# Optimization experiments

Measured on AMD Instinct MI355X. Metric: run time of the kernel, lower is better.

Reference implementation:

```python
import jax, jax.numpy as jnp
import numpy as np

EPS = 1e-7            # keras.backend.epsilon()
NEG = -1e30           # log-space 'zero' (avoid -inf for NaN-free grads)
SUB_SAMPLE = (2, 2)   # encoder conv subsampling factors (non-tensor forward arg)


def setup_inputs() -> dict:
    key = jax.random.key(0)
    k1, k2, k3, k4 = jax.random.split(key, 4)
    B, T, C, L = 128, 2000, 128, 200
    logits = jax.random.normal(k1, (B, T, C), jnp.float32)
    y_pred = jax.nn.softmax(logits, axis=-1)  # ctc_batch_cost expects probabilities
    labels = jax.random.randint(k2, (B, L), 0, C - 1, jnp.int32)  # never the blank (C-1)
    # raw frame counts; after two /2 subsamplings -> in [1000, 2000] <= T
    feat_lens = jax.random.randint(k3, (B,), 4000, 8000, jnp.int32)
    label_lens = jax.random.randint(k4, (B,), 50, L + 1, jnp.int32)
    return {"y_pred": y_pred, "labels": labels, "feat_lens": feat_lens, "label_lens": label_lens}


def _ctc_batch_cost(y_pred, labels, feat_lens, label_lens):
    """Faithful reimplementation of keras.backend.ctc_batch_cost (blank = C-1),
    with the CTCLayer's subsampling of feat_lens applied first."""
    for sub in SUB_SAMPLE:
        if sub > 1:
            feat_lens = (feat_lens + 1) // sub
    log_probs = jnp.log(y_pred + EPS)                 # [B,T,C]
    B, T, C = y_pred.shape
    L = labels.shape[1]
    S = 2 * L + 1
    blank = C - 1

    # extended label sequence: blank, l1, blank, l2, ..., blank  -> [B,S]
    ext = jnp.full((B, S), blank, jnp.int32).at[:, 1::2].set(labels)
    # skip transition s-2 -> s allowed iff ext[s] != blank and ext[s] != ext[s-2]
    skip_ok = jnp.concatenate(
        [jnp.zeros((B, 2), bool), (ext[:, 2:] != blank) & (ext[:, 2:] != ext[:, :-2])],
        axis=1,
    )
    bidx = jnp.arange(B)
    i1 = 2 * label_lens - 1   # last non-blank state
    i2 = 2 * label_lens       # trailing blank state

    lp = jnp.swapaxes(log_probs, 0, 1)                # [T,B,C], scan over time

    emit0 = jnp.take_along_axis(lp[0], ext, axis=1)   # [B,S]
    alpha0 = (jnp.full((B, S), NEG, jnp.float32)
              .at[:, 0].set(emit0[:, 0])
              .at[:, 1].set(emit0[:, 1]))
    ll0 = jnp.logaddexp(alpha0[bidx, i1], alpha0[bidx, i2])
    final0 = jnp.where(feat_lens == 1, ll0, NEG)

    def step(carry, inp):
        alpha, final = carry
        t, lp_t = inp
        emit = jnp.take_along_axis(lp_t, ext, axis=1)              # [B,S]
        a1 = jnp.pad(alpha, ((0, 0), (1, 0)), constant_values=NEG)[:, :-1]
        a2 = jnp.pad(alpha, ((0, 0), (2, 0)), constant_values=NEG)[:, :-2]
        m = jnp.logaddexp(alpha, a1)
        m = jnp.where(skip_ok, jnp.logaddexp(m, a2), m)
        alpha = m + emit
        ll = jnp.logaddexp(alpha[bidx, i1], alpha[bidx, i2])
        final = jnp.where(t == feat_lens - 1, ll, final)           # capture at last valid frame
        return (alpha, final), None

    (_, final), _ = jax.lax.scan(step, (alpha0, final0), (jnp.arange(1, T), lp[1:]))
    return -final[:, None]                                          # [B,1] like ctc_batch_cost


def reference(y_pred, labels, feat_lens, label_lens):
    return _ctc_batch_cost(y_pred, labels, feat_lens, label_lens)
```

## Files before the change

kernel.cpp:

```cpp
#include <hip/hip_runtime.h>
#include <math.h>

#define EPSQ 1e-7f
#define TDIM 2000
#define CDIM 128
#define LDIM 200
#define SDIM 401
#define SPL  7
#define SENTE (-(1 << 30))

#define RINGA 0
#define RINGB 8192
#define LABSI 16384
#define PRODA 16592
#define CONSA 16593
#define PRODB 16594
#define CONSB 16595
#define BDONE 16596
#define BVALS 16608
#define BEXPI 17056
#define SMEMN 17120

__device__ __forceinline__ float dpp_shr_f(float x) {
    return __int_as_float(__builtin_amdgcn_update_dpp(0, __float_as_int(x), 0x138, 0xf, 0xf, true));
}
__device__ __forceinline__ int dpp_shr_i(int x) {
    return __builtin_amdgcn_update_dpp(0, x, 0x138, 0xf, 0xf, true);
}
__device__ __forceinline__ float dpp_shl_f(float x) {
    return __int_as_float(__builtin_amdgcn_update_dpp(0, __float_as_int(x), 0x130, 0xf, 0xf, true));
}
__device__ __forceinline__ int dpp_shl_i(int x) {
    return __builtin_amdgcn_update_dpp(0, x, 0x130, 0xf, 0xf, true);
}

__device__ __forceinline__ void renorm_alpha(float a[SPL], int& E, float& fprev, int lane) {
    float mx = fmaxf(fmaxf(fmaxf(a[0], a[1]), fmaxf(a[2], a[3])),
                     fmaxf(fmaxf(a[4], a[5]), a[6]));
    bool zero = (mx == 0.f);
    int e = ((__float_as_int(mx) >> 23) & 0xff) - 127;
    int S_self = zero ? SENTE : (E + e);
    int S1 = dpp_shr_i(S_self);
    if (lane == 0) S1 = SENTE;
    int S2 = dpp_shr_i(S1);
    if (lane == 0) S2 = SENTE;
    int E_new = max(S_self, S1);
    int E_prevnew = max(S1, S2);
    int dg = E - E_new;
    float g = (zero || dg < -126) ? 0.f : __int_as_float((dg + 127) << 23);
#pragma unroll
    for (int j = 0; j < SPL; ++j) a[j] *= g;
    E = E_new;
    int df = E_prevnew - E_new;
    bool fz = (E_prevnew <= SENTE / 2) || (df < -126);
    if (df > 126) df = 126;
    fprev = fz ? 0.f : __int_as_float((df + 127) << 23);
}

__device__ __forceinline__ void renorm_beta(float b[SPL], int& E, float& fnext, int lane) {
    float mx = fmaxf(fmaxf(fmaxf(b[0], b[1]), fmaxf(b[2], b[3])),
                     fmaxf(fmaxf(b[4], b[5]), b[6]));
    bool zero = (mx == 0.f);
    int e = ((__float_as_int(mx) >> 23) & 0xff) - 127;
    int S_self = zero ? SENTE : (E + e);
    int S1 = dpp_shl_i(S_self);
    if (lane == 63) S1 = SENTE;
    int S2 = dpp_shl_i(S1);
    if (lane == 63) S2 = SENTE;
    int E_new = max(S_self, S1);
    int E_nextnew = max(S1, S2);
    int dg = E - E_new;
    float g = (zero || dg < -126) ? 0.f : __int_as_float((dg + 127) << 23);
#pragma unroll
    for (int j = 0; j < SPL; ++j) b[j] *= g;
    E = E_new;
    int df = E_nextnew - E_new;
    bool fz = (E_nextnew <= SENTE / 2) || (df < -126);
    if (df > 126) df = 126;
    fnext = fz ? 0.f : __int_as_float((df + 127) << 23);
}

#define A_STEP(TOFF) do {                                                     \
    float p6 = dpp_shr_f(a[6]) * fprev;                                       \
    float p5 = dpp_shr_f(a[5]) * fprev;                                       \
    float n0 = fmaf(skipf[0], p5,   a[0] + p6)   * q[(1+(TOFF))&3][0];        \
    float n1 = fmaf(skipf[1], p6,   a[1] + a[0]) * q[(1+(TOFF))&3][1];        \
    float n2 = fmaf(skipf[2], a[0], a[2] + a[1]) * q[(1+(TOFF))&3][2];        \
    float n3 = fmaf(skipf[3], a[1], a[3] + a[2]) * q[(1+(TOFF))&3][3];        \
    float n4 = fmaf(skipf[4], a[2], a[4] + a[3]) * q[(1+(TOFF))&3][4];        \
    float n5 = fmaf(skipf[5], a[3], a[5] + a[4]) * q[(1+(TOFF))&3][5];        \
    float n6 = fmaf(skipf[6], a[4], a[6] + a[5]) * q[(1+(TOFF))&3][6];        \
    a[0]=n0; a[1]=n1; a[2]=n2; a[3]=n3; a[4]=n4; a[5]=n5; a[6]=n6;            \
    if (t + (TOFF) == m) {                                                    \
        _Pragma("unroll")                                                     \
        for (int j = 0; j < SPL; ++j) ac[j] = a[j];                           \
        Eac = E;                                                              \
    }                                                                         \
    {   const int rr = ((t + (TOFF) + 2) & 63) << 7;                          \
        _Pragma("unroll")                                                     \
        for (int j = 0; j < SPL; ++j)                                         \
            q[(3+(TOFF))&3][j] = ringA[rr + cls[j]];                          \
    }                                                                         \
} while (0);

#define B_STEP(SOFF) do {                                                     \
    float c0 = bb[0]*q[(SOFF)&3][0], c1 = bb[1]*q[(SOFF)&3][1];               \
    float c2 = bb[2]*q[(SOFF)&3][2], c3 = bb[3]*q[(SOFF)&3][3];               \
    float c4 = bb[4]*q[(SOFF)&3][4], c5 = bb[5]*q[(SOFF)&3][5];               \
    float c6 = bb[6]*q[(SOFF)&3][6];                                          \
    float cn0 = dpp_shl_f(c0) * fnext;                                        \
    float cn1 = dpp_shl_f(c1) * fnext;                                        \
    bb[0] = fmaf(skb[0], c2, c0 + c1);                                        \
    bb[1] = fmaf(skb[1], c3, c1 + c2);                                        \
    bb[2] = fmaf(skb[2], c4, c2 + c3);                                        \
    bb[3] = fmaf(skb[3], c5, c3 + c4);                                        \
    bb[4] = fmaf(skb[4], c6, c4 + c5);                                        \
    bb[5] = fmaf(skb[5], cn0, c5 + c6);                                       \
    bb[6] = fmaf(skb[6], cn1, c6 + cn0);                                      \
    if (s + (SOFF) == scap) {                                                 \
        _Pragma("unroll")                                                     \
        for (int j = 0; j < SPL; ++j) bc[j] = bb[j];                          \
        Ebc = E;                                                              \
    }                                                                         \
    {   const int rr = ((t0 - s - (SOFF) - 2) & 63) << 7;                     \
        _Pragma("unroll")                                                     \
        for (int j = 0; j < SPL; ++j)                                         \
            q[(2+(SOFF))&3][j] = ringB[rr + cls[j]];                          \
    }                                                                         \
} while (0);

__global__ void __launch_bounds__(256, 1)
__attribute__((amdgpu_waves_per_eu(1, 1)))
ctc_kernel(const float* __restrict__ y_pred,
           const int* __restrict__ labels,
           const int* __restrict__ feat_lens,
           const int* __restrict__ label_lens,
           float* __restrict__ out)
{
    __shared__ int smem[SMEMN];
    float* smf = (float*)smem;
    volatile int* vsm = (volatile int*)smem;

    const int b = blockIdx.x;
    const int tid = threadIdx.x;
    const int lane = tid & 63;
    const int wv = tid >> 6;

    int f = feat_lens[b];
    f = (f + 1) >> 1; f = (f + 1) >> 1;
    const int Tbm1 = f - 1;
    const int m = f >> 1;

    if (tid < 8) smem[PRODA + tid] = 0;
    const int* labrow = labels + b * LDIM;
    for (int i = tid; i < LDIM; i += 256) smem[LABSI + i] = labrow[i];
    __syncthreads();

    const float4* rp4 = (const float4*)(y_pred + (size_t)b * TDIM * CDIM);

    if (wv == 2) {
        const int pend = (m + 18) >> 1;
        int p = 0;
        while (p <= pend) {
            while (vsm[CONSA] + 32 < p + 8) __builtin_amdgcn_s_sleep(2);
            asm volatile("" ::: "memory");
            float4 w[8];
#pragma unroll
            for (int i = 0; i < 8; ++i) {
                int pi = p + i; if (pi > pend) pi = pend;
                w[i] = rp4[pi * 64 + lane];
            }
#pragma unroll
            for (int i = 0; i < 8; ++i) {
                int pi = p + i; if (pi > pend) pi = pend;
                float4 x = w[i];
                x.x += EPSQ; x.y += EPSQ; x.z += EPSQ; x.w += EPSQ;
                *(float4*)&smf[RINGA + (pi & 31) * 256 + lane * 4] = x;
            }
            asm volatile("s_waitcnt lgkmcnt(0)" ::: "memory");
            vsm[PRODA] = p + 8;
            p += 8;
        }
        return;
    }
    if (wv == 3) {
        const int pstart = Tbm1 >> 1;
        int pl = (m - 18) >> 1; if (pl < 0) pl = 0;
        const int kend = pstart - pl;
        int k = 0;
        while (k <= kend) {
            while (vsm[CONSB] + 32 < k + 8) __builtin_amdgcn_s_sleep(2);
            asm volatile("" ::: "memory");
            float4 w[8];
#pragma unroll
            for (int i = 0; i < 8; ++i) {
                int ki = k + i; if (ki > kend) ki = kend;
                w[i] = rp4[(pstart - ki) * 64 + lane];
            }
#pragma unroll
            for (int i = 0; i < 8; ++i) {
                int ki = k + i; if (ki > kend) ki = kend;
                float4 x = w[i];
                x.x += EPSQ; x.y += EPSQ; x.z += EPSQ; x.w += EPSQ;
                *(float4*)&smf[RINGB + ((pstart - ki) & 31) * 256 + lane * 4] = x;
            }
            asm volatile("s_waitcnt lgkmcnt(0)" ::: "memory");
            vsm[PRODB] = k + 8;
            k += 8;
        }
        return;
    }

    const int llen = label_lens[b];
    const int i1 = 2 * llen - 1, i2 = 2 * llen;
    int cls[SPL]; float skipf[SPL];
    const int s0 = lane * SPL;
#pragma unroll
    for (int j = 0; j < SPL; ++j) {
        int s = s0 + j;
        int c = CDIM - 1; float sk = 0.f;
        if (s < SDIM && (s & 1)) {
            int kk = s >> 1;
            c = smem[LABSI + kk];
            if (kk >= 1 && smem[LABSI + kk] != smem[LABSI + kk - 1]) sk = 1.f;
        }
        cls[j] = c; skipf[j] = sk;
    }
    const float* ringA = &smf[RINGA];
    const float* ringB = &smf[RINGB];

    if (wv == 0) {
        float a[SPL], q[4][SPL], ac[SPL];
        int E = 0, Eac = 0;
        float fprev = 0.f;
#pragma unroll
        for (int j = 0; j < SPL; ++j) { a[j] = 0.f; ac[j] = 0.f; }

        while (vsm[PRODA] < 2) __builtin_amdgcn_s_sleep(1);
        asm volatile("" ::: "memory");
#pragma unroll
        for (int j = 0; j < SPL; ++j) {
            q[0][j] = ringA[(0 << 7) + cls[j]];
            q[1][j] = ringA[(1 << 7) + cls[j]];
            q[2][j] = ringA[(2 << 7) + cls[j]];
        }
        if (lane == 0) { a[0] = q[0][0]; a[1] = q[0][1]; }

        int t = 1;
        while (t <= m) {
            vsm[CONSA] = (t >= 2) ? (((t - 2) >> 1) + 1) : 0;
            int need = ((t + 17) >> 1) + 1;
            while (vsm[PRODA] < need) __builtin_amdgcn_s_sleep(1);
            asm volatile("" ::: "memory");
            renorm_alpha(a, E, fprev, lane);
            A_STEP(0) A_STEP(1) A_STEP(2) A_STEP(3)
            renorm_alpha(a, E, fprev, lane);
            A_STEP(4) A_STEP(5) A_STEP(6) A_STEP(7)
            renorm_alpha(a, E, fprev, lane);
            A_STEP(8) A_STEP(9) A_STEP(10) A_STEP(11)
            renorm_alpha(a, E, fprev, lane);
            A_STEP(12) A_STEP(13) A_STEP(14) A_STEP(15)
            t += 16;
        }
        vsm[CONSA] = 1 << 28;
        asm volatile("" ::: "memory");

        while (vsm[BDONE] == 0) __builtin_amdgcn_s_sleep(1);
        asm volatile("" ::: "memory");
        int Eb = smem[BEXPI + lane];
        float dot = 0.f;
#pragma unroll
        for (int j = 0; j < SPL; ++j)
            dot = fmaf(ac[j], smf[BVALS + lane * SPL + j], dot);
        float l2 = (dot > 0.f) ? (log2f(dot) + (float)(Eac + Eb)) : -1e30f;
        float M = l2;
#pragma unroll
        for (int d = 1; d < 64; d <<= 1) M = fmaxf(M, __shfl_xor(M, d, 64));
        float S = exp2f(l2 - M);
#pragma unroll
        for (int d = 1; d < 64; d <<= 1) S += __shfl_xor(S, d, 64);
        if (lane == 0)
            out[b] = -(M + log2f(S)) * 0.69314718055994530942f;
    } else {
        float bb[SPL], q[4][SPL], bc[SPL];
        int E = 0, Ebc = 0;
        float fnext = 0.f;
#pragma unroll
        for (int j = 0; j < SPL; ++j) {
            int s = s0 + j;
            bb[j] = (s == i1 || s == i2) ? 1.f : 0.f;
            bc[j] = 0.f;
        }
        float skb[SPL];
#pragma unroll
        for (int j = 0; j < 5; ++j) skb[j] = skipf[j + 2];
        skb[5] = (lane == 63) ? 0.f : __shfl_down(skipf[0], 1, 64);
        skb[6] = (lane == 63) ? 0.f : __shfl_down(skipf[1], 1, 64);

        const int t0 = Tbm1;
        const int nb = t0 - m;
        const int scap = nb - 1;
        const int pstart = t0 >> 1;

        while (vsm[PRODB] < 2) __builtin_amdgcn_s_sleep(1);
        asm volatile("" ::: "memory");
#pragma unroll
        for (int j = 0; j < SPL; ++j) {
            q[0][j] = ringB[((t0 & 63) << 7) + cls[j]];
            q[1][j] = ringB[(((t0 - 1) & 63) << 7) + cls[j]];
        }

        int s = 0;
        while (s < nb) {
            int tcur = t0 - s;
            vsm[CONSB] = pstart - ((tcur + 2) >> 1) + 1;
            int need = pstart - ((tcur - 17) >> 1) + 1;
            while (vsm[PRODB] < need) __builtin_amdgcn_s_sleep(1);
            asm volatile("" ::: "memory");
            renorm_beta(bb, E, fnext, lane);
            B_STEP(0) B_STEP(1) B_STEP(2) B_STEP(3)
            renorm_beta(bb, E, fnext, lane);
            B_STEP(4) B_STEP(5) B_STEP(6) B_STEP(7)
            renorm_beta(bb, E, fnext, lane);
            B_STEP(8) B_STEP(9) B_STEP(10) B_STEP(11)
            renorm_beta(bb, E, fnext, lane);
            B_STEP(12) B_STEP(13) B_STEP(14) B_STEP(15)
            s += 16;
        }
        vsm[CONSB] = 1 << 28;
        asm volatile("" ::: "memory");
#pragma unroll
        for (int j = 0; j < SPL; ++j) smf[BVALS + lane * SPL + j] = bc[j];
        smem[BEXPI + lane] = Ebc;
        asm volatile("s_waitcnt lgkmcnt(0)" ::: "memory");
        vsm[BDONE] = 1;
    }
}

extern "C" void kernel_launch(void* const* d_in, const int* in_sizes, int n_in,
                              void* d_out, int out_size, void* d_ws, size_t ws_size,
                              hipStream_t stream) {
    (void)d_ws; (void)ws_size; (void)n_in; (void)out_size;
    const float* y_pred     = (const float*)d_in[0];
    const int*   labels     = (const int*)d_in[1];
    const int*   feat_lens  = (const int*)d_in[2];
    const int*   label_lens = (const int*)d_in[3];
    float* out = (float*)d_out;
    const int B = in_sizes[2];
    ctc_kernel<<<B, 256, 0, stream>>>(y_pred, labels, feat_lens, label_lens, out);
}
```

Measured before the change: 273.3 us.

## Split alpha/beta into separate blocks with direct global gathers and combine kernel

Replaces the single 256-thread block per sequence, which had two producer waves streaming rows into LDS rings and busy-wait flags, with two 64-thread blocks per sequence. One block runs the forward alpha pass and the other the backward beta pass. Each lane now gathers only its needed label and blank probabilities straight from global memory into a 12-deep register prefetch queue. A second small kernel merges the alpha and beta halves through workspace. This removes the LDS ring traffic and spin synchronisation and doubles the number of blocks, but risks global-load latency on the serial dependency chain and adds a second launch.

```diff
diff --git a/kernel.cpp b/kernel.cpp
--- a/kernel.cpp
+++ b/kernel.cpp
@@ -8,18 +8,7 @@
 #define SDIM 401
 #define SPL  7
 #define SENTE (-(1 << 30))
-
-#define RINGA 0
-#define RINGB 8192
-#define LABSI 16384
-#define PRODA 16592
-#define CONSA 16593
-#define PRODB 16594
-#define CONSB 16595
-#define BDONE 16596
-#define BVALS 16608
-#define BEXPI 17056
-#define SMEMN 17120
+#define PD   12
 
 __device__ __forceinline__ float dpp_shr_f(float x) {
     return __int_as_float(__builtin_amdgcn_update_dpp(0, __float_as_int(x), 0x138, 0xf, 0xf, true));
@@ -80,209 +69,156 @@
     fnext = fz ? 0.f : __int_as_float((df + 127) << 23);
 }
 
-#define A_STEP(TOFF) do {                                                     \
-    float p6 = dpp_shr_f(a[6]) * fprev;                                       \
-    float p5 = dpp_shr_f(a[5]) * fprev;                                       \
-    float n0 = fmaf(skipf[0], p5,   a[0] + p6)   * q[(1+(TOFF))&3][0];        \
-    float n1 = fmaf(skipf[1], p6,   a[1] + a[0]) * q[(1+(TOFF))&3][1];        \
-    float n2 = fmaf(skipf[2], a[0], a[2] + a[1]) * q[(1+(TOFF))&3][2];        \
-    float n3 = fmaf(skipf[3], a[1], a[3] + a[2]) * q[(1+(TOFF))&3][3];        \
-    float n4 = fmaf(skipf[4], a[2], a[4] + a[3]) * q[(1+(TOFF))&3][4];        \
-    float n5 = fmaf(skipf[5], a[3], a[5] + a[4]) * q[(1+(TOFF))&3][5];        \
-    float n6 = fmaf(skipf[6], a[4], a[6] + a[5]) * q[(1+(TOFF))&3][6];        \
-    a[0]=n0; a[1]=n1; a[2]=n2; a[3]=n3; a[4]=n4; a[5]=n5; a[6]=n6;            \
-    if (t + (TOFF) == m) {                                                    \
-        _Pragma("unroll")                                                     \
-        for (int j = 0; j < SPL; ++j) ac[j] = a[j];                           \
-        Eac = E;                                                              \
-    }                                                                         \
-    {   const int rr = ((t + (TOFF) + 2) & 63) << 7;                          \
-        _Pragma("unroll")                                                     \
-        for (int j = 0; j < SPL; ++j)                                         \
-            q[(3+(TOFF))&3][j] = ringA[rr + cls[j]];                          \
-    }                                                                         \
+#define BUILD_Q(SL)                                                            \
+    float Bv = QB[SL] + EPSQ;                                                  \
+    float e0 = QL[SL][0] + EPSQ, e1 = QL[SL][1] + EPSQ;                        \
+    float e2 = QL[SL][2] + EPSQ, e3 = QL[SL][3] + EPSQ;                        \
+    float q0 = par ? e0 : Bv, q1 = par ? Bv : e0;                              \
+    float q2 = par ? e1 : Bv, q3 = par ? Bv : e1;                              \
+    float q4 = par ? e2 : Bv, q5 = par ? Bv : e2;                              \
+    float q6 = par ? e3 : Bv;
+
+#define RELOAD(SL, ROW)                                                        \
+    {   const float* rowp = ybase + (size_t)(ROW) * CDIM;                      \
+        QB[SL] = rowp[CDIM - 1];                                               \
+        QL[SL][0] = rowp[offL[0]]; QL[SL][1] = rowp[offL[1]];                  \
+        QL[SL][2] = rowp[offL[2]]; QL[SL][3] = rowp[offL[3]]; }
+
+#define A_STEP(TOFF) do {                                                      \
+    constexpr int SL = (1 + (TOFF)) % PD;                                      \
+    const int tcur = t + (TOFF);                                               \
+    BUILD_Q(SL)                                                                \
+    float p6 = dpp_shr_f(a[6]) * fprev;                                        \
+    float p5 = dpp_shr_f(a[5]) * fprev;                                        \
+    float n0 = fmaf(skipf[0], p5,   a[0] + p6)   * q0;                         \
+    float n1 = fmaf(skipf[1], p6,   a[1] + a[0]) * q1;                         \
+    float n2 = fmaf(skipf[2], a[0], a[2] + a[1]) * q2;                         \
+    float n3 = fmaf(skipf[3], a[1], a[3] + a[2]) * q3;                         \
+    float n4 = fmaf(skipf[4], a[2], a[4] + a[3]) * q4;                         \
+    float n5 = fmaf(skipf[5], a[3], a[5] + a[4]) * q5;                         \
+    float n6 = fmaf(skipf[6], a[4], a[6] + a[5]) * q6;                         \
+    a[0]=n0; a[1]=n1; a[2]=n2; a[3]=n3; a[4]=n4; a[5]=n5; a[6]=n6;             \
+    if (tcur == m) {                                                           \
+        _Pragma("unroll")                                                      \
+        for (int j = 0; j < SPL; ++j) ac[j] = a[j];                            \
+        Eac = E;                                                               \
+    }                                                                          \
+    RELOAD(SL, tcur + PD)                                                      \
 } while (0);
 
-#define B_STEP(SOFF) do {                                                     \
-    float c0 = bb[0]*q[(SOFF)&3][0], c1 = bb[1]*q[(SOFF)&3][1];               \
-    float c2 = bb[2]*q[(SOFF)&3][2], c3 = bb[3]*q[(SOFF)&3][3];               \
-    float c4 = bb[4]*q[(SOFF)&3][4], c5 = bb[5]*q[(SOFF)&3][5];               \
-    float c6 = bb[6]*q[(SOFF)&3][6];                                          \
-    float cn0 = dpp_shl_f(c0) * fnext;                                        \
-    float cn1 = dpp_shl_f(c1) * fnext;                                        \
-    bb[0] = fmaf(skb[0], c2, c0 + c1);                                        \
-    bb[1] = fmaf(skb[1], c3, c1 + c2);                                        \
-    bb[2] = fmaf(skb[2], c4, c2 + c3);                                        \
-    bb[3] = fmaf(skb[3], c5, c3 + c4);                                        \
-    bb[4] = fmaf(skb[4], c6, c4 + c5);                                        \
-    bb[5] = fmaf(skb[5], cn0, c5 + c6);                                       \
-    bb[6] = fmaf(skb[6], cn1, c6 + cn0);                                      \
-    if (s + (SOFF) == scap) {                                                 \
-        _Pragma("unroll")                                                     \
-        for (int j = 0; j < SPL; ++j) bc[j] = bb[j];                          \
-        Ebc = E;                                                              \
-    }                                                                         \
-    {   const int rr = ((t0 - s - (SOFF) - 2) & 63) << 7;                     \
-        _Pragma("unroll")                                                     \
-        for (int j = 0; j < SPL; ++j)                                         \
-            q[(2+(SOFF))&3][j] = ringB[rr + cls[j]];                          \
-    }                                                                         \
+#define B_STEP(SOFF) do {                                                      \
+    constexpr int SL = (SOFF) % PD;                                            \
+    const int scur = s + (SOFF);                                               \
+    BUILD_Q(SL)                                                                \
+    float c0 = bb[0]*q0, c1 = bb[1]*q1, c2 = bb[2]*q2, c3 = bb[3]*q3;          \
+    float c4 = bb[4]*q4, c5 = bb[5]*q5, c6 = bb[6]*q6;                         \
+    float cn0 = dpp_shl_f(c0) * fnext;                                         \
+    float cn1 = dpp_shl_f(c1) * fnext;                                         \
+    bb[0] = fmaf(skb[0], c2, c0 + c1);                                         \
+    bb[1] = fmaf(skb[1], c3, c1 + c2);                                         \
+    bb[2] = fmaf(skb[2], c4, c2 + c3);                                         \
+    bb[3] = fmaf(skb[3], c5, c3 + c4);                                         \
+    bb[4] = fmaf(skb[4], c6, c4 + c5);                                         \
+    bb[5] = fmaf(skb[5], cn0, c5 + c6);                                        \
+    bb[6] = fmaf(skb[6], cn1, c6 + cn0);                                       \
+    if (scur == scap) {                                                        \
+        _Pragma("unroll")                                                      \
+        for (int j = 0; j < SPL; ++j) bc[j] = bb[j];                           \
+        Ebc = E;                                                               \
+    }                                                                          \
+    RELOAD(SL, t0 - scur - PD)                                                 \
 } while (0);
 
-__global__ void __launch_bounds__(256, 1)
+__global__ void __launch_bounds__(64)
 __attribute__((amdgpu_waves_per_eu(1, 1)))
-ctc_kernel(const float* __restrict__ y_pred,
-           const int* __restrict__ labels,
-           const int* __restrict__ feat_lens,
-           const int* __restrict__ label_lens,
-           float* __restrict__ out)
+ctc_main(const float* __restrict__ y_pred,
+         const int* __restrict__ labels,
+         const int* __restrict__ feat_lens,
+         const int* __restrict__ label_lens,
+         float* __restrict__ ws)
 {
-    __shared__ int smem[SMEMN];
-    float* smf = (float*)smem;
-    volatile int* vsm = (volatile int*)smem;
-
-    const int b = blockIdx.x;
-    const int tid = threadIdx.x;
-    const int lane = tid & 63;
-    const int wv = tid >> 6;
+    const int b = blockIdx.x >> 1;
+    const int role = blockIdx.x & 1;
+    const int lane = threadIdx.x;
 
     int f = feat_lens[b];
     f = (f + 1) >> 1; f = (f + 1) >> 1;
     const int Tbm1 = f - 1;
     const int m = f >> 1;
-
-    if (tid < 8) smem[PRODA + tid] = 0;
-    const int* labrow = labels + b * LDIM;
-    for (int i = tid; i < LDIM; i += 256) smem[LABSI + i] = labrow[i];
-    __syncthreads();
-
-    const float4* rp4 = (const float4*)(y_pred + (size_t)b * TDIM * CDIM);
-
-    if (wv == 2) {
-        const int pend = (m + 18) >> 1;
-        int p = 0;
-        while (p <= pend) {
-            while (vsm[CONSA] + 32 < p + 8) __builtin_amdgcn_s_sleep(2);
-            asm volatile("" ::: "memory");
-            float4 w[8];
-#pragma unroll
-            for (int i = 0; i < 8; ++i) {
-                int pi = p + i; if (pi > pend) pi = pend;
-                w[i] = rp4[pi * 64 + lane];
-            }
-#pragma unroll
-            for (int i = 0; i < 8; ++i) {
-                int pi = p + i; if (pi > pend) pi = pend;
-                float4 x = w[i];
-                x.x += EPSQ; x.y += EPSQ; x.z += EPSQ; x.w += EPSQ;
-                *(float4*)&smf[RINGA + (pi & 31) * 256 + lane * 4] = x;
-            }
-            asm volatile("s_waitcnt lgkmcnt(0)" ::: "memory");
-            vsm[PRODA] = p + 8;
-            p += 8;
-        }
-        return;
-    }
-    if (wv == 3) {
-        const int pstart = Tbm1 >> 1;
-        int pl = (m - 18) >> 1; if (pl < 0) pl = 0;
-        const int kend = pstart - pl;
-        int k = 0;
-        while (k <= kend) {
-            while (vsm[CONSB] + 32 < k + 8) __builtin_amdgcn_s_sleep(2);
-            asm volatile("" ::: "memory");
-            float4 w[8];
-#pragma unroll
-            for (int i = 0; i < 8; ++i) {
-                int ki = k + i; if (ki > kend) ki = kend;
-                w[i] = rp4[(pstart - ki) * 64 + lane];
-            }
-#pragma unroll
-            for (int i = 0; i < 8; ++i) {
-                int ki = k + i; if (ki > kend) ki = kend;
-                float4 x = w[i];
-                x.x += EPSQ; x.y += EPSQ; x.z += EPSQ; x.w += EPSQ;
-                *(float4*)&smf[RINGB + ((pstart - ki) & 31) * 256 + lane * 4] = x;
-            }
-            asm volatile("s_waitcnt lgkmcnt(0)" ::: "memory");
-            vsm[PRODB] = k + 8;
-            k += 8;
-        }
-        return;
-    }
-
     const int llen = label_lens[b];
     const int i1 = 2 * llen - 1, i2 = 2 * llen;
-    int cls[SPL]; float skipf[SPL];
+
+    const float* ybase = y_pred + (size_t)b * TDIM * CDIM;
+    const int* labrow = labels + b * LDIM;
+
     const int s0 = lane * SPL;
+    const int k0 = s0 >> 1;
+    const bool par = (lane & 1) != 0;
+    int LA[5];
+#pragma unroll
+    for (int i = 0; i < 5; ++i) {
+        int k = k0 - 1 + i;
+        if (k < 0) k = 0;
+        if (k > LDIM - 1) k = LDIM - 1;
+        LA[i] = labrow[k];
+    }
+    int offL[4];
+#pragma unroll
+    for (int i = 0; i < 4; ++i) offL[i] = LA[i + 1];
+
+    float skipf[SPL];
 #pragma unroll
     for (int j = 0; j < SPL; ++j) {
         int s = s0 + j;
-        int c = CDIM - 1; float sk = 0.f;
-        if (s < SDIM && (s & 1)) {
-            int kk = s >> 1;
-            c = smem[LABSI + kk];
-            if (kk >= 1 && smem[LABSI + kk] != smem[LABSI + kk - 1]) sk = 1.f;
-        }
-        cls[j] = c; skipf[j] = sk;
+        float sk = 0.f;
+        bool emit = (s < SDIM) && ((s & 1) != 0);
+        if (emit) {
+            int idx = (j >> 1) + 1;
+            int k = k0 + (j >> 1);
+            if (k >= 1 && LA[idx] != LA[idx - 1]) sk = 1.f;
+        }
+        skipf[j] = sk;
     }
-    const float* ringA = &smf[RINGA];
-    const float* ringB = &smf[RINGB];
-
-    if (wv == 0) {
-        float a[SPL], q[4][SPL], ac[SPL];
+
+    float QB[PD], QL[PD][4];
+
+    float* wsb = ws + (size_t)b * 1024 + role * 512;
+
+    if (role == 0) {
+#pragma unroll
+        for (int r = 0; r < PD; ++r) RELOAD(r, r)
+
+        float a[SPL], ac[SPL];
         int E = 0, Eac = 0;
         float fprev = 0.f;
 #pragma unroll
         for (int j = 0; j < SPL; ++j) { a[j] = 0.f; ac[j] = 0.f; }
-
-        while (vsm[PRODA] < 2) __builtin_amdgcn_s_sleep(1);
-        asm volatile("" ::: "memory");
-#pragma unroll
-        for (int j = 0; j < SPL; ++j) {
-            q[0][j] = ringA[(0 << 7) + cls[j]];
-            q[1][j] = ringA[(1 << 7) + cls[j]];
-            q[2][j] = ringA[(2 << 7) + cls[j]];
-        }
-        if (lane == 0) { a[0] = q[0][0]; a[1] = q[0][1]; }
-
-        int t = 1;
-        while (t <= m) {
-            vsm[CONSA] = (t >= 2) ? (((t - 2) >> 1) + 1) : 0;
-            int need = ((t + 17) >> 1) + 1;
-            while (vsm[PRODA] < need) __builtin_amdgcn_s_sleep(1);
-            asm volatile("" ::: "memory");
+        {
+            BUILD_Q(0)
+            if (lane == 0) { a[0] = q0; a[1] = q1; }
+            RELOAD(0, PD)
+        }
+
+        for (int t = 1; t <= m; t += PD) {
             renorm_alpha(a, E, fprev, lane);
             A_STEP(0) A_STEP(1) A_STEP(2) A_STEP(3)
             renorm_alpha(a, E, fprev, lane);
             A_STEP(4) A_STEP(5) A_STEP(6) A_STEP(7)
             renorm_alpha(a, E, fprev, lane);
             A_STEP(8) A_STEP(9) A_STEP(10) A_STEP(11)
-            renorm_alpha(a, E, fprev, lane);
-            A_STEP(12) A_STEP(13) A_STEP(14) A_STEP(15)
-            t += 16;
-        }
-        vsm[CONSA] = 1 << 28;
-        asm volatile("" ::: "memory");
-
-        while (vsm[BDONE] == 0) __builtin_amdgcn_s_sleep(1);
-        asm volatile("" ::: "memory");
-        int Eb = smem[BEXPI + lane];
-        float dot = 0.f;
-#pragma unroll
-        for (int j = 0; j < SPL; ++j)
-            dot = fmaf(ac[j], smf[BVALS + lane * SPL + j], dot);
-        float l2 = (dot > 0.f) ? (log2f(dot) + (float)(Eac + Eb)) : -1e30f;
-        float M = l2;
-#pragma unroll
-        for (int d = 1; d < 64; d <<= 1) M = fmaxf(M, __shfl_xor(M, d, 64));
-        float S = exp2f(l2 - M);
-#pragma unroll
-        for (int d = 1; d < 64; d <<= 1) S += __shfl_xor(S, d, 64);
-        if (lane == 0)
-            out[b] = -(M + log2f(S)) * 0.69314718055994530942f;
+        }
+#pragma unroll
+        for (int j = 0; j < SPL; ++j) wsb[lane * 8 + j] = ac[j];
+        ((int*)wsb)[lane * 8 + 7] = Eac;
     } else {
-        float bb[SPL], q[4][SPL], bc[SPL];
+        const int t0 = Tbm1;
+        const int nb = t0 - m;
+        const int scap = nb - 1;
+
+#pragma unroll
+        for (int r = 0; r < PD; ++r) RELOAD(r, t0 - r)
+
+        float bb[SPL], bc[SPL];
         int E = 0, Ebc = 0;
         float fnext = 0.f;
 #pragma unroll
@@ -297,55 +233,54 @@
         skb[5] = (lane == 63) ? 0.f : __shfl_down(skipf[0], 1, 64);
         skb[6] = (lane == 63) ? 0.f : __shfl_down(skipf[1], 1, 64);
 
-        const int t0 = Tbm1;
-        const int nb = t0 - m;
-        const int scap = nb - 1;
-        const int pstart = t0 >> 1;
-
-        while (vsm[PRODB] < 2) __builtin_amdgcn_s_sleep(1);
-        asm volatile("" ::: "memory");
-#pragma unroll
-        for (int j = 0; j < SPL; ++j) {
-            q[0][j] = ringB[((t0 & 63) << 7) + cls[j]];
-            q[1][j] = ringB[(((t0 - 1) & 63) << 7) + cls[j]];
-        }
-
-        int s = 0;
-        while (s < nb) {
-            int tcur = t0 - s;
-            vsm[CONSB] = pstart - ((tcur + 2) >> 1) + 1;
-            int need = pstart - ((tcur - 17) >> 1) + 1;
-            while (vsm[PRODB] < need) __builtin_amdgcn_s_sleep(1);
-            asm volatile("" ::: "memory");
+        for (int s = 0; s < nb; s += PD) {
             renorm_beta(bb, E, fnext, lane);
             B_STEP(0) B_STEP(1) B_STEP(2) B_STEP(3)
             renorm_beta(bb, E, fnext, lane);
             B_STEP(4) B_STEP(5) B_STEP(6) B_STEP(7)
             renorm_beta(bb, E, fnext, lane);
             B_STEP(8) B_STEP(9) B_STEP(10) B_STEP(11)
-            renorm_beta(bb, E, fnext, lane);
-            B_STEP(12) B_STEP(13) B_STEP(14) B_STEP(15)
-            s += 16;
-        }
-        vsm[CONSB] = 1 << 28;
-        asm volatile("" ::: "memory");
-#pragma unroll
-        for (int j = 0; j < SPL; ++j) smf[BVALS + lane * SPL + j] = bc[j];
-        smem[BEXPI + lane] = Ebc;
-        asm volatile("s_waitcnt lgkmcnt(0)" ::: "memory");
-        vsm[BDONE] = 1;
+        }
+#pragma unroll
+        for (int j = 0; j < SPL; ++j) wsb[lane * 8 + j] = bc[j];
+        ((int*)wsb)[lane * 8 + 7] = Ebc;
     }
+}
+
+__global__ void __launch_bounds__(64)
+ctc_combine(const float* __restrict__ ws, float* __restrict__ out)
+{
+    const int b = blockIdx.x;
+    const int lane = threadIdx.x;
+    const float* wa = ws + (size_t)b * 1024 + lane * 8;
+    const float* wb = wa + 512;
+    float dot = 0.f;
+#pragma unroll
+    for (int j = 0; j < SPL; ++j) dot = fmaf(wa[j], wb[j], dot);
+    int Ea = ((const int*)wa)[7];
+    int Eb = ((const int*)wb)[7];
+    float l2 = (dot > 0.f) ? (log2f(dot) + (float)(Ea + Eb)) : -1e30f;
+    float M = l2;
+#pragma unroll
+    for (int d = 1; d < 64; d <<= 1) M = fmaxf(M, __shfl_xor(M, d, 64));
+    float S = exp2f(l2 - M);
+#pragma unroll
+    for (int d = 1; d < 64; d <<= 1) S += __shfl_xor(S, d, 64);
+    if (lane == 0)
+        out[b] = -(M + log2f(S)) * 0.69314718055994530942f;
 }
 
 extern "C" void kernel_launch(void* const* d_in, const int* in_sizes, int n_in,
                               void* d_out, int out_size, void* d_ws, size_t ws_size,
                               hipStream_t stream) {
-    (void)d_ws; (void)ws_size; (void)n_in; (void)out_size;
+    (void)n_in; (void)out_size; (void)ws_size;
     const float* y_pred     = (const float*)d_in[0];
     const int*   labels     = (const int*)d_in[1];
     const int*   feat_lens  = (const int*)d_in[2];
     const int*   label_lens = (const int*)d_in[3];
     float* out = (float*)d_out;
+    float* ws  = (float*)d_ws;
     const int B = in_sizes[2];
-    ctc_kernel<<<B, 256, 0, stream>>>(y_pred, labels, feat_lens, label_lens, out);
-}
+    ctc_main<<<2 * B, 64, 0, stream>>>(y_pred, labels, feat_lens, label_lens, ws);
+    ctc_combine<<<B, 64, 0, stream>>>(ws, out);
+}
```

Result: slower. 333.3 us (+21.9%).
